# Kernel tuning notes

Measured on AMD Instinct MI355X. Metric: run time of the kernel, lower is better.

Reference implementation:

```python
import jax, jax.numpy as jnp
import numpy as np


def setup_inputs() -> dict:
    key = jax.random.key(0)
    k1, k2, k3 = jax.random.split(key, 3)
    B, T, D, H = 64, 512, 1024, 1024
    x = jax.random.normal(k1, (B, T, D), dtype=jnp.float32)
    state = jnp.zeros((B, H), dtype=jnp.float32)
    W = jax.random.normal(k2, (H, H), dtype=jnp.float32) / np.sqrt(H).astype(np.float32)
    U = jax.random.normal(k3, (D, H), dtype=jnp.float32) / np.sqrt(D).astype(np.float32)
    b = jnp.zeros((H,), dtype=jnp.float32)
    return {"x": x, "state": state, "W": W, "U": U, "b": b}


def reference(x, state, W, U, b):
    # x: (B, T, D) -> precompute input projection for all steps: (T, B, H)
    xU = jnp.einsum('btd,dh->tbh', x, U) + b

    def step(h, xu_t):
        h = jnp.tanh(xu_t + h @ W)
        return h, h

    final_state, outs = jax.lax.scan(step, state, xU)  # outs: (T, B, H)
    outs = jnp.transpose(outs, (1, 0, 2))  # (B, T, H)
    return outs, final_state
```

## Files before the change

### kernel.cpp

```cpp
#include <hip/hip_runtime.h>
#include <hip/hip_fp16.h>

typedef float  f4v __attribute__((ext_vector_type(4)));
typedef _Float16 h8v __attribute__((ext_vector_type(8)));
typedef _Float16 h4v __attribute__((ext_vector_type(4)));
typedef unsigned uv4 __attribute__((ext_vector_type(4)));

#define B_ 64
#define T_ 512
#define H_ 1024

__global__ __launch_bounds__(256) void k_transpose_cvt(const float* __restrict__ src,
                                                       _Float16* __restrict__ dst) {
  __shared__ _Float16 tile[64][72];
  int r0 = blockIdx.y * 64, c0 = blockIdx.x * 64;
  int t = threadIdx.x;
  for (int i = 0; i < 4; ++i) {
    int r = i * 16 + (t >> 4);
    int c = (t & 15) * 4;
    f4v v = *reinterpret_cast<const f4v*>(src + (long)(r0 + r) * 1024 + c0 + c);
    tile[c + 0][r] = (_Float16)v.x;
    tile[c + 1][r] = (_Float16)v.y;
    tile[c + 2][r] = (_Float16)v.z;
    tile[c + 3][r] = (_Float16)v.w;
  }
  __syncthreads();
  for (int i = 0; i < 2; ++i) {
    int rr = i * 32 + (t >> 3);
    int cc = (t & 7) * 8;
    *reinterpret_cast<h8v*>(dst + (long)(c0 + rr) * 1024 + r0 + cc) =
        *reinterpret_cast<const h8v*>(&tile[rr][cc]);
  }
}

#define SWZG(r, kh) ((((r) * 64) + ((kh) * 2)) ^ (((r) & 3) << 4))

__global__ __launch_bounds__(256) void k_gemm_xu(const float* __restrict__ x,
                                                 const _Float16* __restrict__ Ut,
                                                 const float* __restrict__ bias,
                                                 float* __restrict__ out) {
  __shared__ __attribute__((aligned(16))) unsigned char Asm[128 * 32 * 2];
  __shared__ __attribute__((aligned(16))) unsigned char Bsm[128 * 32 * 2];
  int bid = blockIdx.x;
  int nt = bid & 7, mt = bid >> 3;
  int t = threadIdx.x;
  int row = t >> 1, kc = (t & 1) * 16;
  long gA = (long)(mt * 128 + row) * 1024 + kc;
  long gB = (long)(nt * 128 + row) * 1024 + kc;
  int wid = t >> 6, lane = t & 63;
  int wr = (wid >> 1) * 64, wc = (wid & 1) * 64;
  int l15 = lane & 15, khi = (lane >> 4) * 8;

  f4v acc[4][4];
  for (int i = 0; i < 4; ++i)
    for (int j = 0; j < 4; ++j) acc[i][j] = (f4v){0.f, 0.f, 0.f, 0.f};

  f4v ra[4];
  h8v rb[2];
  {
    const float* ap = x + gA;
    ra[0] = *(const f4v*)(ap);     ra[1] = *(const f4v*)(ap + 4);
    ra[2] = *(const f4v*)(ap + 8); ra[3] = *(const f4v*)(ap + 12);
    const _Float16* bp = Ut + gB;
    rb[0] = *(const h8v*)(bp);     rb[1] = *(const h8v*)(bp + 8);
  }
  for (int kt = 0; kt < 32; ++kt) {
    h8v ah0, ah1;
    for (int j = 0; j < 4; ++j) {
      ah0[j]     = (_Float16)ra[0][j];
      ah0[j + 4] = (_Float16)ra[1][j];
      ah1[j]     = (_Float16)ra[2][j];
      ah1[j + 4] = (_Float16)ra[3][j];
    }
    *(h8v*)(Asm + SWZG(row, kc))     = ah0;
    *(h8v*)(Asm + SWZG(row, kc + 8)) = ah1;
    *(h8v*)(Bsm + SWZG(row, kc))     = rb[0];
    *(h8v*)(Bsm + SWZG(row, kc + 8)) = rb[1];
    __syncthreads();
    if (kt < 31) {
      const float* ap = x + gA + (kt + 1) * 32;
      ra[0] = *(const f4v*)(ap);     ra[1] = *(const f4v*)(ap + 4);
      ra[2] = *(const f4v*)(ap + 8); ra[3] = *(const f4v*)(ap + 12);
      const _Float16* bp = Ut + gB + (kt + 1) * 32;
      rb[0] = *(const h8v*)(bp);     rb[1] = *(const h8v*)(bp + 8);
    }
    h8v af[4], bf[4];
    for (int mi = 0; mi < 4; ++mi)
      af[mi] = *(const h8v*)(Asm + SWZG(wr + mi * 16 + l15, khi));
    for (int ni = 0; ni < 4; ++ni)
      bf[ni] = *(const h8v*)(Bsm + SWZG(wc + ni * 16 + l15, khi));
    for (int mi = 0; mi < 4; ++mi)
      for (int ni = 0; ni < 4; ++ni)
        acc[mi][ni] = __builtin_amdgcn_mfma_f32_16x16x32_f16(af[mi], bf[ni], acc[mi][ni], 0, 0, 0);
    __syncthreads();
  }
  int coff = nt * 128 + wc, roff = mt * 128 + wr;
  for (int ni = 0; ni < 4; ++ni) {
    int col = coff + ni * 16 + l15;
    float bb = bias[col];
    for (int mi = 0; mi < 4; ++mi) {
      int rbase = roff + mi * 16 + (lane >> 4) * 4;
      for (int j = 0; j < 4; ++j)
        out[(long)(rbase + j) * 1024 + col] = acc[mi][ni][j] + bb;
    }
  }
}

#define SWZS(r, kh) ((((r) * 2048) + ((kh) * 2)) ^ (((r) & 7) << 4))

static __device__ __forceinline__ _Float16 lo_h(unsigned u) {
  unsigned short s = (unsigned short)u;
  _Float16 h;
  __builtin_memcpy(&h, &s, 2);
  return h;
}
static __device__ __forceinline__ unsigned pk(float f, unsigned tg) {
  _Float16 h = (_Float16)f;
  unsigned short s;
  __builtin_memcpy(&s, &h, 2);
  return (tg << 16) | (unsigned)s;
}

__global__ __launch_bounds__(256) void k_scan(const float* __restrict__ state,
                                              float* __restrict__ out,
                                              const _Float16* __restrict__ Wt,
                                              unsigned* __restrict__ hx,
                                              unsigned* __restrict__ ctr) {
  extern __shared__ __attribute__((aligned(16))) unsigned char smem[];
  unsigned char* Wl = smem;
  unsigned char* Hl = smem + 65536;
  int t = threadIdx.x;
  int bid = blockIdx.x;
  int cl = bid & 7;
  int mm = bid >> 3;
  int lane = t & 63;

  unsigned* stepc = ctr + cl * 32;

  {
    int r = t >> 3, c8 = t & 7;
    const _Float16* wsrc = Wt + (long)(mm * 32 + r) * 1024;
    for (int j = 0; j < 16; ++j) {
      int kh = (c8 + 8 * j) * 8;
      *(h8v*)(Wl + SWZS(r, kh)) = *(const h8v*)(wsrc + kh);
    }
  }

  int wid = t >> 6;
  int srow = t >> 5, slane = t & 31;
  long b = cl * 8 + srow;
  int l15 = lane & 15, khi8 = (lane >> 4) * 8;
  int arow = lane & 7;
  int bro = wid * 16 + l15;
  int hi = lane >> 4;
  int gcol = mm * 32 + wid * 16 + l15;
  bool prod = (wid < 2) && (hi < 2);

  for (int step = 0; step < T_; ++step) {
    float xuv[4];
    long addr0 = 0;
    if (prod) {
      addr0 = ((long)(cl * 8 + hi * 4) * T_ + step) * 1024 + gcol;
#pragma unroll
      for (int j = 0; j < 4; ++j) xuv[j] = out[addr0 + (long)j * T_ * 1024];
    }

    if (step == 0) {
      const float* hp0 = state + b * 1024 + slane * 4;
#pragma unroll
      for (int j = 0; j < 8; ++j) {
        f4v v = *(const f4v*)(hp0 + 128 * j);
        h4v hv = {(_Float16)v.x, (_Float16)v.y, (_Float16)v.z, (_Float16)v.w};
        *(h4v*)(Hl + SWZS(srow, (slane + 32 * j) * 4)) = hv;
      }
    } else {
      if (t == 0) {
        unsigned tgt = 32u * (unsigned)step;
        while (__hip_atomic_load(stepc, __ATOMIC_RELAXED, __HIP_MEMORY_SCOPE_AGENT) < tgt)
          __builtin_amdgcn_s_sleep(1);
      }
      __syncthreads();

      const unsigned* hp = hx + (((step - 1) & 1) * 64 + b) * 1024 + slane * 4;
      unsigned tg = (unsigned)(step - 1);
      uv4 c0, c1, c2, c3, c4, c5, c6, c7;
      for (;;) {
        asm volatile(
            "global_load_dwordx4 %0, %8, off sc0 sc1\n\t"
            "global_load_dwordx4 %1, %8, off offset:512 sc0 sc1\n\t"
            "global_load_dwordx4 %2, %8, off offset:1024 sc0 sc1\n\t"
            "global_load_dwordx4 %3, %8, off offset:1536 sc0 sc1\n\t"
            "global_load_dwordx4 %4, %8, off offset:2048 sc0 sc1\n\t"
            "global_load_dwordx4 %5, %8, off offset:2560 sc0 sc1\n\t"
            "global_load_dwordx4 %6, %8, off offset:3072 sc0 sc1\n\t"
            "global_load_dwordx4 %7, %8, off offset:3584 sc0 sc1\n\t"
            "s_waitcnt vmcnt(0)"
            : "=&v"(c0), "=&v"(c1), "=&v"(c2), "=&v"(c3),
              "=&v"(c4), "=&v"(c5), "=&v"(c6), "=&v"(c7)
            : "v"(hp)
            : "memory");
        unsigned d =
            (((c0.x >> 16) ^ tg) | ((c0.y >> 16) ^ tg) | ((c0.z >> 16) ^ tg) | ((c0.w >> 16) ^ tg)) |
            (((c1.x >> 16) ^ tg) | ((c1.y >> 16) ^ tg) | ((c1.z >> 16) ^ tg) | ((c1.w >> 16) ^ tg)) |
            (((c2.x >> 16) ^ tg) | ((c2.y >> 16) ^ tg) | ((c2.z >> 16) ^ tg) | ((c2.w >> 16) ^ tg)) |
            (((c3.x >> 16) ^ tg) | ((c3.y >> 16) ^ tg) | ((c3.z >> 16) ^ tg) | ((c3.w >> 16) ^ tg)) |
            (((c4.x >> 16) ^ tg) | ((c4.y >> 16) ^ tg) | ((c4.z >> 16) ^ tg) | ((c4.w >> 16) ^ tg)) |
            (((c5.x >> 16) ^ tg) | ((c5.y >> 16) ^ tg) | ((c5.z >> 16) ^ tg) | ((c5.w >> 16) ^ tg)) |
            (((c6.x >> 16) ^ tg) | ((c6.y >> 16) ^ tg) | ((c6.z >> 16) ^ tg) | ((c6.w >> 16) ^ tg)) |
            (((c7.x >> 16) ^ tg) | ((c7.y >> 16) ^ tg) | ((c7.z >> 16) ^ tg) | ((c7.w >> 16) ^ tg));
        if (d == 0u) break;
      }
      {
        uv4 cc[8] = {c0, c1, c2, c3, c4, c5, c6, c7};
#pragma unroll
        for (int j = 0; j < 8; ++j) {
          h4v hv = {lo_h(cc[j].x), lo_h(cc[j].y), lo_h(cc[j].z), lo_h(cc[j].w)};
          *(h4v*)(Hl + SWZS(srow, (slane + 32 * j) * 4)) = hv;
        }
      }
    }
    __syncthreads();

    if (wid < 2) {
      f4v ac0 = (f4v){0.f, 0.f, 0.f, 0.f}, ac1 = ac0, ac2 = ac0, ac3 = ac0;
#pragma unroll
      for (int s = 0; s < 32; s += 4) {
        int k0 = s * 32 + khi8, k1 = k0 + 32, k2 = k0 + 64, k3 = k0 + 96;
        h8v af0 = *(const h8v*)(Hl + SWZS(arow, k0));
        h8v bf0 = *(const h8v*)(Wl + SWZS(bro, k0));
        h8v af1 = *(const h8v*)(Hl + SWZS(arow, k1));
        h8v bf1 = *(const h8v*)(Wl + SWZS(bro, k1));
        h8v af2 = *(const h8v*)(Hl + SWZS(arow, k2));
        h8v bf2 = *(const h8v*)(Wl + SWZS(bro, k2));
        h8v af3 = *(const h8v*)(Hl + SWZS(arow, k3));
        h8v bf3 = *(const h8v*)(Wl + SWZS(bro, k3));
        ac0 = __builtin_amdgcn_mfma_f32_16x16x32_f16(af0, bf0, ac0, 0, 0, 0);
        ac1 = __builtin_amdgcn_mfma_f32_16x16x32_f16(af1, bf1, ac1, 0, 0, 0);
        ac2 = __builtin_amdgcn_mfma_f32_16x16x32_f16(af2, bf2, ac2, 0, 0, 0);
        ac3 = __builtin_amdgcn_mfma_f32_16x16x32_f16(af3, bf3, ac3, 0, 0, 0);
      }
      f4v acc = (ac0 + ac1) + (ac2 + ac3);
      if (hi < 2) {
        float v0 = tanhf(acc[0] + xuv[0]);
        float v1 = tanhf(acc[1] + xuv[1]);
        float v2 = tanhf(acc[2] + xuv[2]);
        float v3 = tanhf(acc[3] + xuv[3]);
        if (step < T_ - 1) {
          unsigned u0 = pk(v0, (unsigned)step), u1 = pk(v1, (unsigned)step);
          unsigned u2 = pk(v2, (unsigned)step), u3 = pk(v3, (unsigned)step);
          unsigned* q0 = hx + ((long)(step & 1) * 64 + cl * 8 + hi * 4) * 1024 + gcol;
          unsigned* q1 = q0 + 1024;
          unsigned* q2 = q0 + 2048;
          unsigned* q3 = q0 + 3072;
          asm volatile(
              "global_store_dword %0, %4, off sc0 sc1\n\t"
              "global_store_dword %1, %5, off sc0 sc1\n\t"
              "global_store_dword %2, %6, off sc0 sc1\n\t"
              "global_store_dword %3, %7, off sc0 sc1"
              :: "v"(q0), "v"(q1), "v"(q2), "v"(q3),
                 "v"(u0), "v"(u1), "v"(u2), "v"(u3)
              : "memory");
        }
        out[addr0]                   = v0;
        out[addr0 + (long)T_ * 1024] = v1;
        out[addr0 + (long)T_ * 2048] = v2;
        out[addr0 + (long)T_ * 3072] = v3;
        if (step == T_ - 1) {
          long r = (long)cl * 8 + hi * 4;
          float* q = out + (long)B_ * T_ * 1024 + r * 1024 + gcol;
          q[0] = v0; q[1024] = v1; q[2048] = v2; q[3072] = v3;
        }
      }
    }

    __syncthreads();
    if (t == 0 && step < T_ - 1) {
      __hip_atomic_fetch_add(stepc, 1u, __ATOMIC_RELAXED, __HIP_MEMORY_SCOPE_AGENT);
    }
  }
}

extern "C" void kernel_launch(void* const* d_in, const int* in_sizes, int n_in,
                              void* d_out, int out_size, void* d_ws, size_t ws_size,
                              hipStream_t stream) {
  const float* x     = (const float*)d_in[0];
  const float* state = (const float*)d_in[1];
  const float* W     = (const float*)d_in[2];
  const float* U     = (const float*)d_in[3];
  const float* bias  = (const float*)d_in[4];
  float* out = (float*)d_out;
  unsigned char* ws = (unsigned char*)d_ws;

  _Float16* Ut = (_Float16*)ws;
  _Float16* Wt = (_Float16*)(ws + (1u << 21));
  unsigned* hx  = (unsigned*)ws;
  unsigned* ctr = (unsigned*)(ws + (1u << 22));

  hipMemsetAsync(ctr, 0, 4096, stream);

  k_transpose_cvt<<<dim3(16, 16), 256, 0, stream>>>(U, Ut);
  k_transpose_cvt<<<dim3(16, 16), 256, 0, stream>>>(W, Wt);
  k_gemm_xu<<<2048, 256, 0, stream>>>(x, Ut, bias, out);

  hipMemsetAsync(hx, 0xFF, 2u * 64u * 1024u * 4u, stream);

  hipFuncSetAttribute((const void*)k_scan, hipFuncAttributeMaxDynamicSharedMemorySize, 81920);
  void* args[] = {(void*)&state, (void*)&out, (void*)&Wt, (void*)&hx, (void*)&ctr};
  hipLaunchCooperativeKernel((void*)k_scan, dim3(256), dim3(256), args, 81920, stream);
}
```

Measured before the change: 1.663 ms.

## Replace per-step counter wait with clock-deadline polling and deeper hidden-state ring

Blocks first meet at a one-time global barrier to agree on a shared realtime-clock base. At each step the per-cluster counter wait ends early once a per-step deadline on that clock passes, and correctness is left to the existing tag-checked polling of the hidden-state buffer. The hidden-state exchange buffer grows from 2 to 4 slots so producers can run ahead. A guard makes sure step-2 has finished before a slot is reused. The aim is to take the counter round-trip off the critical path of the serial scan, at the cost of extra polling traffic, a hand-tuned clock constant and more complex synchronisation.

```diff
diff --git a/kernel.cpp b/kernel.cpp
--- a/kernel.cpp
+++ b/kernel.cpp
@@ -9,6 +9,8 @@
 #define B_ 64
 #define T_ 512
 #define H_ 1024
+#define DELTA_TICKS 180LL
+#define HX_DEPTH 4
 
 __global__ __launch_bounds__(256) void k_transpose_cvt(const float* __restrict__ src,
                                                        _Float16* __restrict__ dst) {
@@ -129,6 +131,8 @@
   extern __shared__ __attribute__((aligned(16))) unsigned char smem[];
   unsigned char* Wl = smem;
   unsigned char* Hl = smem + 65536;
+  __shared__ long long baseS;
+  __shared__ int guardok;
   int t = threadIdx.x;
   int bid = blockIdx.x;
   int cl = bid & 7;
@@ -136,6 +140,7 @@
   int lane = t & 63;
 
   unsigned* stepc = ctr + cl * 32;
+  unsigned* gbar  = ctr + 512;
 
   {
     int r = t >> 3, c8 = t & 7;
@@ -145,6 +150,17 @@
       *(h8v*)(Wl + SWZS(r, kh)) = *(const h8v*)(wsrc + kh);
     }
   }
+
+  if (t == 0) {
+    __hip_atomic_fetch_add(gbar, 1u, __ATOMIC_RELAXED, __HIP_MEMORY_SCOPE_AGENT);
+    while (__hip_atomic_load(gbar, __ATOMIC_RELAXED, __HIP_MEMORY_SCOPE_AGENT) < 256u)
+      __builtin_amdgcn_s_sleep(2);
+    unsigned long long rt = __builtin_amdgcn_s_memrealtime();
+    baseS = (long long)(((rt >> 8) + 2) << 8);
+    guardok = 1;
+  }
+  __syncthreads();
+  const long long base = baseS;
 
   int wid = t >> 6;
   int srow = t >> 5, slane = t & 31;
@@ -173,15 +189,29 @@
         h4v hv = {(_Float16)v.x, (_Float16)v.y, (_Float16)v.z, (_Float16)v.w};
         *(h4v*)(Hl + SWZS(srow, (slane + 32 * j) * 4)) = hv;
       }
+      __syncthreads();
     } else {
       if (t == 0) {
+        long long tau = base + (long long)step * DELTA_TICKS;
         unsigned tgt = 32u * (unsigned)step;
-        while (__hip_atomic_load(stepc, __ATOMIC_RELAXED, __HIP_MEMORY_SCOPE_AGENT) < tgt)
-          __builtin_amdgcn_s_sleep(1);
+        for (;;) {
+          long long rt = (long long)__builtin_amdgcn_s_memrealtime();
+          if (rt - tau >= 0) break;
+          if (__hip_atomic_load(stepc, __ATOMIC_RELAXED, __HIP_MEMORY_SCOPE_AGENT) >= tgt)
+            break;
+          __builtin_amdgcn_s_sleep(2);
+        }
+        guardok = 1;
+        if (step >= 3) {
+          unsigned need = 32u * (unsigned)(step - 2);
+          if (__hip_atomic_load(stepc, __ATOMIC_RELAXED, __HIP_MEMORY_SCOPE_AGENT) < need)
+            guardok = 0;
+        }
       }
       __syncthreads();
 
-      const unsigned* hp = hx + (((step - 1) & 1) * 64 + b) * 1024 + slane * 4;
+      const unsigned* hp =
+          hx + (((step - 1) & (HX_DEPTH - 1)) * 64 + b) * 1024 + slane * 4;
       unsigned tg = (unsigned)(step - 1);
       uv4 c0, c1, c2, c3, c4, c5, c6, c7;
       for (;;) {
@@ -209,6 +239,7 @@
             (((c6.x >> 16) ^ tg) | ((c6.y >> 16) ^ tg) | ((c6.z >> 16) ^ tg) | ((c6.w >> 16) ^ tg)) |
             (((c7.x >> 16) ^ tg) | ((c7.y >> 16) ^ tg) | ((c7.z >> 16) ^ tg) | ((c7.w >> 16) ^ tg));
         if (d == 0u) break;
+        __builtin_amdgcn_s_sleep(2);
       }
       {
         uv4 cc[8] = {c0, c1, c2, c3, c4, c5, c6, c7};
@@ -218,8 +249,16 @@
           *(h4v*)(Hl + SWZS(srow, (slane + 32 * j) * 4)) = hv;
         }
       }
-    }
-    __syncthreads();
+      __syncthreads();
+      if (!guardok) {
+        if (t == 0) {
+          unsigned need = 32u * (unsigned)(step - 2);
+          while (__hip_atomic_load(stepc, __ATOMIC_RELAXED, __HIP_MEMORY_SCOPE_AGENT) < need)
+            __builtin_amdgcn_s_sleep(2);
+        }
+        __syncthreads();
+      }
+    }
 
     if (wid < 2) {
       f4v ac0 = (f4v){0.f, 0.f, 0.f, 0.f}, ac1 = ac0, ac2 = ac0, ac3 = ac0;
@@ -248,7 +287,7 @@
         if (step < T_ - 1) {
           unsigned u0 = pk(v0, (unsigned)step), u1 = pk(v1, (unsigned)step);
           unsigned u2 = pk(v2, (unsigned)step), u3 = pk(v3, (unsigned)step);
-          unsigned* q0 = hx + ((long)(step & 1) * 64 + cl * 8 + hi * 4) * 1024 + gcol;
+          unsigned* q0 = hx + ((long)(step & (HX_DEPTH - 1)) * 64 + cl * 8 + hi * 4) * 1024 + gcol;
           unsigned* q1 = q0 + 1024;
           unsigned* q2 = q0 + 2048;
           unsigned* q3 = q0 + 3072;
@@ -302,7 +341,7 @@
   k_transpose_cvt<<<dim3(16, 16), 256, 0, stream>>>(W, Wt);
   k_gemm_xu<<<2048, 256, 0, stream>>>(x, Ut, bias, out);
 
-  hipMemsetAsync(hx, 0xFF, 2u * 64u * 1024u * 4u, stream);
+  hipMemsetAsync(hx, 0xFF, (size_t)HX_DEPTH * 64u * 1024u * 4u, stream);
 
   hipFuncSetAttribute((const void*)k_scan, hipFuncAttributeMaxDynamicSharedMemorySize, 81920);
   void* args[] = {(void*)&state, (void*)&out, (void*)&Wt, (void*)&hx, (void*)&ctr};
```

Result: slower. 1.739 ms (+4.5%).

## Replace per-step counter barrier with tag polling and cached fast-path exchange

Applied to the files above, without the earlier changes.

Drops the per-cluster atomic step counter and its wait and increment. Consumers now poll the tagged hidden-state buffer directly, and the exchange buffers are quadruple-buffered. At start-up a probe checks whether all blocks of a cluster can see each other's plain (non-sc) stores through a shared cache. If they can, producers also write a second copy with plain stores, and consumers try cheap cached loads a few times before falling back to the coherent sc0 sc1 path. This aims to cut barrier latency and L2-bypass load latency on the serial critical path, but it relies on cache-visibility assumptions checked only heuristically and adds extra stores.

```diff
diff --git a/kernel.cpp b/kernel.cpp
--- a/kernel.cpp
+++ b/kernel.cpp
@@ -121,21 +121,49 @@
   return (tg << 16) | (unsigned)s;
 }
 
+#define TAGBAD(tg)                                                                             \
+  ((((c0.x >> 16) ^ (tg)) | ((c0.y >> 16) ^ (tg)) | ((c0.z >> 16) ^ (tg)) | ((c0.w >> 16) ^ (tg))) | \
+   (((c1.x >> 16) ^ (tg)) | ((c1.y >> 16) ^ (tg)) | ((c1.z >> 16) ^ (tg)) | ((c1.w >> 16) ^ (tg))) | \
+   (((c2.x >> 16) ^ (tg)) | ((c2.y >> 16) ^ (tg)) | ((c2.z >> 16) ^ (tg)) | ((c2.w >> 16) ^ (tg))) | \
+   (((c3.x >> 16) ^ (tg)) | ((c3.y >> 16) ^ (tg)) | ((c3.z >> 16) ^ (tg)) | ((c3.w >> 16) ^ (tg))) | \
+   (((c4.x >> 16) ^ (tg)) | ((c4.y >> 16) ^ (tg)) | ((c4.z >> 16) ^ (tg)) | ((c4.w >> 16) ^ (tg))) | \
+   (((c5.x >> 16) ^ (tg)) | ((c5.y >> 16) ^ (tg)) | ((c5.z >> 16) ^ (tg)) | ((c5.w >> 16) ^ (tg))) | \
+   (((c6.x >> 16) ^ (tg)) | ((c6.y >> 16) ^ (tg)) | ((c6.z >> 16) ^ (tg)) | ((c6.w >> 16) ^ (tg))) | \
+   (((c7.x >> 16) ^ (tg)) | ((c7.y >> 16) ^ (tg)) | ((c7.z >> 16) ^ (tg)) | ((c7.w >> 16) ^ (tg))))
+
+#define LOAD8(PTR, FLAGS)                                                 \
+  asm volatile(                                                           \
+      "global_load_dwordx4 %0, %8, off " FLAGS "\n\t"                     \
+      "global_load_dwordx4 %1, %8, off offset:512 " FLAGS "\n\t"          \
+      "global_load_dwordx4 %2, %8, off offset:1024 " FLAGS "\n\t"         \
+      "global_load_dwordx4 %3, %8, off offset:1536 " FLAGS "\n\t"         \
+      "global_load_dwordx4 %4, %8, off offset:2048 " FLAGS "\n\t"         \
+      "global_load_dwordx4 %5, %8, off offset:2560 " FLAGS "\n\t"         \
+      "global_load_dwordx4 %6, %8, off offset:3072 " FLAGS "\n\t"         \
+      "global_load_dwordx4 %7, %8, off offset:3584 " FLAGS "\n\t"         \
+      "s_waitcnt vmcnt(0)"                                                \
+      : "=&v"(c0), "=&v"(c1), "=&v"(c2), "=&v"(c3),                       \
+        "=&v"(c4), "=&v"(c5), "=&v"(c6), "=&v"(c7)                        \
+      : "v"(PTR)                                                          \
+      : "memory")
+
 __global__ __launch_bounds__(256) void k_scan(const float* __restrict__ state,
                                               float* __restrict__ out,
                                               const _Float16* __restrict__ Wt,
                                               unsigned* __restrict__ hx,
+                                              unsigned* __restrict__ hx2,
                                               unsigned* __restrict__ ctr) {
   extern __shared__ __attribute__((aligned(16))) unsigned char smem[];
   unsigned char* Wl = smem;
   unsigned char* Hl = smem + 65536;
+  __shared__ int fastflag;
   int t = threadIdx.x;
   int bid = blockIdx.x;
   int cl = bid & 7;
   int mm = bid >> 3;
   int lane = t & 63;
 
-  unsigned* stepc = ctr + cl * 32;
+  unsigned* gbar = ctr + 512;
 
   {
     int r = t >> 3, c8 = t & 7;
@@ -145,6 +173,32 @@
       *(h8v*)(Wl + SWZS(r, kh)) = *(const h8v*)(wsrc + kh);
     }
   }
+
+  if (t == 0) {
+    unsigned* tst = ctr + 1024 + bid * 32;
+    unsigned val = 0xC0FFEE00u + (unsigned)bid;
+    asm volatile("global_store_dword %0, %1, off\n\ts_waitcnt vmcnt(0)"
+                 :: "v"(tst), "v"(val) : "memory");
+    __hip_atomic_fetch_add(gbar, 1u, __ATOMIC_RELAXED, __HIP_MEMORY_SCOPE_AGENT);
+    while (__hip_atomic_load(gbar, __ATOMIC_RELAXED, __HIP_MEMORY_SCOPE_AGENT) < 256u)
+      __builtin_amdgcn_s_sleep(2);
+  }
+  __syncthreads();
+  if (t < 64) {
+    bool ok = true;
+    if (lane < 32) {
+      int peer = lane * 8 + cl;
+      unsigned* ps = ctr + 1024 + peer * 32;
+      unsigned v;
+      asm volatile("global_load_dword %0, %1, off\n\ts_waitcnt vmcnt(0)"
+                   : "=v"(v) : "v"(ps) : "memory");
+      ok = (v == 0xC0FFEE00u + (unsigned)peer);
+    }
+    unsigned long long m = __ballot(ok);
+    if (t == 0) fastflag = (m == ~0ULL);
+  }
+  __syncthreads();
+  const bool fastm = (fastflag != 0);
 
   int wid = t >> 6;
   int srow = t >> 5, slane = t & 31;
@@ -174,41 +228,24 @@
         *(h4v*)(Hl + SWZS(srow, (slane + 32 * j) * 4)) = hv;
       }
     } else {
-      if (t == 0) {
-        unsigned tgt = 32u * (unsigned)step;
-        while (__hip_atomic_load(stepc, __ATOMIC_RELAXED, __HIP_MEMORY_SCOPE_AGENT) < tgt)
-          __builtin_amdgcn_s_sleep(1);
-      }
-      __syncthreads();
-
-      const unsigned* hp = hx + (((step - 1) & 1) * 64 + b) * 1024 + slane * 4;
       unsigned tg = (unsigned)(step - 1);
+      long roff = ((long)((step - 1) & 3) * 64 + b) * 1024 + slane * 4;
+      const unsigned* hpF = hx + roff;
+      const unsigned* hpS = hx2 + roff;
       uv4 c0, c1, c2, c3, c4, c5, c6, c7;
-      for (;;) {
-        asm volatile(
-            "global_load_dwordx4 %0, %8, off sc0 sc1\n\t"
-            "global_load_dwordx4 %1, %8, off offset:512 sc0 sc1\n\t"
-            "global_load_dwordx4 %2, %8, off offset:1024 sc0 sc1\n\t"
-            "global_load_dwordx4 %3, %8, off offset:1536 sc0 sc1\n\t"
-            "global_load_dwordx4 %4, %8, off offset:2048 sc0 sc1\n\t"
-            "global_load_dwordx4 %5, %8, off offset:2560 sc0 sc1\n\t"
-            "global_load_dwordx4 %6, %8, off offset:3072 sc0 sc1\n\t"
-            "global_load_dwordx4 %7, %8, off offset:3584 sc0 sc1\n\t"
-            "s_waitcnt vmcnt(0)"
-            : "=&v"(c0), "=&v"(c1), "=&v"(c2), "=&v"(c3),
-              "=&v"(c4), "=&v"(c5), "=&v"(c6), "=&v"(c7)
-            : "v"(hp)
-            : "memory");
-        unsigned d =
-            (((c0.x >> 16) ^ tg) | ((c0.y >> 16) ^ tg) | ((c0.z >> 16) ^ tg) | ((c0.w >> 16) ^ tg)) |
-            (((c1.x >> 16) ^ tg) | ((c1.y >> 16) ^ tg) | ((c1.z >> 16) ^ tg) | ((c1.w >> 16) ^ tg)) |
-            (((c2.x >> 16) ^ tg) | ((c2.y >> 16) ^ tg) | ((c2.z >> 16) ^ tg) | ((c2.w >> 16) ^ tg)) |
-            (((c3.x >> 16) ^ tg) | ((c3.y >> 16) ^ tg) | ((c3.z >> 16) ^ tg) | ((c3.w >> 16) ^ tg)) |
-            (((c4.x >> 16) ^ tg) | ((c4.y >> 16) ^ tg) | ((c4.z >> 16) ^ tg) | ((c4.w >> 16) ^ tg)) |
-            (((c5.x >> 16) ^ tg) | ((c5.y >> 16) ^ tg) | ((c5.z >> 16) ^ tg) | ((c5.w >> 16) ^ tg)) |
-            (((c6.x >> 16) ^ tg) | ((c6.y >> 16) ^ tg) | ((c6.z >> 16) ^ tg) | ((c6.w >> 16) ^ tg)) |
-            (((c7.x >> 16) ^ tg) | ((c7.y >> 16) ^ tg) | ((c7.z >> 16) ^ tg) | ((c7.w >> 16) ^ tg));
-        if (d == 0u) break;
+      bool got = false;
+      if (fastm) {
+#pragma unroll 1
+        for (int tr = 0; tr < 4; ++tr) {
+          LOAD8(hpF, "");
+          if (TAGBAD(tg) == 0u) { got = true; break; }
+          __builtin_amdgcn_s_sleep(2);
+        }
+      }
+      while (!got) {
+        LOAD8(hpS, "sc0 sc1");
+        if (TAGBAD(tg) == 0u) break;
+        __builtin_amdgcn_s_sleep(2);
       }
       {
         uv4 cc[8] = {c0, c1, c2, c3, c4, c5, c6, c7};
@@ -248,7 +285,12 @@
         if (step < T_ - 1) {
           unsigned u0 = pk(v0, (unsigned)step), u1 = pk(v1, (unsigned)step);
           unsigned u2 = pk(v2, (unsigned)step), u3 = pk(v3, (unsigned)step);
-          unsigned* q0 = hx + ((long)(step & 1) * 64 + cl * 8 + hi * 4) * 1024 + gcol;
+          long qoff = ((long)(step & 3) * 64 + cl * 8 + hi * 4) * 1024 + gcol;
+          if (fastm) {
+            unsigned* qF = hx + qoff;
+            qF[0] = u0; qF[1024] = u1; qF[2048] = u2; qF[3072] = u3;
+          }
+          unsigned* q0 = hx2 + qoff;
           unsigned* q1 = q0 + 1024;
           unsigned* q2 = q0 + 2048;
           unsigned* q3 = q0 + 3072;
@@ -274,9 +316,6 @@
     }
 
     __syncthreads();
-    if (t == 0 && step < T_ - 1) {
-      __hip_atomic_fetch_add(stepc, 1u, __ATOMIC_RELAXED, __HIP_MEMORY_SCOPE_AGENT);
-    }
   }
 }
 
@@ -294,17 +333,18 @@
   _Float16* Ut = (_Float16*)ws;
   _Float16* Wt = (_Float16*)(ws + (1u << 21));
   unsigned* hx  = (unsigned*)ws;
+  unsigned* hx2 = (unsigned*)(ws + (1u << 20));
   unsigned* ctr = (unsigned*)(ws + (1u << 22));
 
-  hipMemsetAsync(ctr, 0, 4096, stream);
+  hipMemsetAsync(ctr, 0, 40960, stream);
 
   k_transpose_cvt<<<dim3(16, 16), 256, 0, stream>>>(U, Ut);
   k_transpose_cvt<<<dim3(16, 16), 256, 0, stream>>>(W, Wt);
   k_gemm_xu<<<2048, 256, 0, stream>>>(x, Ut, bias, out);
 
-  hipMemsetAsync(hx, 0xFF, 2u * 64u * 1024u * 4u, stream);
+  hipMemsetAsync(ws, 0xFF, 1u << 21, stream);
 
   hipFuncSetAttribute((const void*)k_scan, hipFuncAttributeMaxDynamicSharedMemorySize, 81920);
-  void* args[] = {(void*)&state, (void*)&out, (void*)&Wt, (void*)&hx, (void*)&ctr};
+  void* args[] = {(void*)&state, (void*)&out, (void*)&Wt, (void*)&hx, (void*)&hx2, (void*)&ctr};
   hipLaunchCooperativeKernel((void*)k_scan, dim3(256), dim3(256), args, 81920, stream);
 }
```

New measurement: 2.320 ms. +39.5%, slower.
